# Performance work log

Hardware: AMD Instinct MI355X
Metric: run time of the kernel (lower is better)

## Reference

```python
import jax, jax.numpy as jnp
import numpy as np

N = 100_000          # nodes
E = 800_000          # edges
IN_DIM = 128
OUT_DIM = 128
H = 8                # heads
DK = OUT_DIM // H    # 16
T = 3                # node types
R = 8                # edge relation types
LN_EPS = 1e-5


def setup_inputs():
    key = jax.random.key(0)
    k = jax.random.split(key, 16)
    node_inp = jax.random.normal(k[0], (N, IN_DIM), dtype=jnp.float32)
    node_type = jax.random.randint(k[1], (N,), 0, T)
    edge_index = jax.random.randint(k[2], (2, E), 0, N)
    edge_type = jax.random.randint(k[3], (E,), 0, R)
    edge_sign = jax.random.randint(k[4], (E,), 0, 3) - 1      # values in {-1,0,1}
    edge_distance = jax.random.uniform(k[5], (E,), dtype=jnp.float32) * 2e5
    sc = 1.0 / np.sqrt(IN_DIM)
    Wq = jax.random.normal(k[6], (T, IN_DIM, OUT_DIM), dtype=jnp.float32) * sc
    Wk = jax.random.normal(k[7], (T, IN_DIM, OUT_DIM), dtype=jnp.float32) * sc
    Wv = jax.random.normal(k[8], (T, IN_DIM, OUT_DIM), dtype=jnp.float32) * sc
    bq = jnp.zeros((T, OUT_DIM), jnp.float32)
    bk = jnp.zeros((T, OUT_DIM), jnp.float32)
    bv = jnp.zeros((T, OUT_DIM), jnp.float32)
    rel_q = jax.random.normal(k[9], (R, H, DK), dtype=jnp.float32) * 0.2
    rel_k = jax.random.normal(k[10], (R, H, DK), dtype=jnp.float32) * 0.2
    rel_v = jax.random.normal(k[11], (R, H, DK), dtype=jnp.float32) * 0.2
    rel_bias = jnp.zeros((R, H), jnp.float32)
    ones = jnp.ones((H, DK), dtype=jnp.float32)
    sign_k_fixed = jnp.stack([-ones, ones], axis=0)   # [2,H,DK] buffers (neg,pos)
    sign_v_fixed = jnp.stack([-ones, ones], axis=0)
    sign_k_neutral = jnp.ones((H, DK), jnp.float32)
    sign_v_neutral = jnp.ones((H, DK), jnp.float32)
    dist_alpha = jnp.float32(0.1)
    dist_tau = jnp.float32(1e5)
    skip = jnp.ones((T,), jnp.float32)
    ln_gamma = jnp.ones((T, OUT_DIM), jnp.float32)
    ln_beta = jnp.zeros((T, OUT_DIM), jnp.float32)
    return dict(node_inp=node_inp, node_type=node_type, edge_index=edge_index,
                edge_type=edge_type, edge_sign=edge_sign, edge_distance=edge_distance,
                Wq=Wq, bq=bq, Wk=Wk, bk=bk, Wv=Wv, bv=bv,
                rel_q=rel_q, rel_k=rel_k, rel_v=rel_v, rel_bias=rel_bias,
                sign_k_fixed=sign_k_fixed, sign_v_fixed=sign_v_fixed,
                sign_k_neutral=sign_k_neutral, sign_v_neutral=sign_v_neutral,
                dist_alpha=dist_alpha, dist_tau=dist_tau, skip=skip,
                ln_gamma=ln_gamma, ln_beta=ln_beta)


def reference(node_inp, node_type, edge_index, edge_type, edge_sign, edge_distance,
              Wq, bq, Wk, bk, Wv, bv, rel_q, rel_k, rel_v, rel_bias,
              sign_k_fixed, sign_v_fixed, sign_k_neutral, sign_v_neutral,
              dist_alpha, dist_tau, skip, ln_gamma, ln_beta):
    src, dst = edge_index[0], edge_index[1]
    n = node_inp.shape[0]
    e = src.shape[0]
    # Per-node-type Q/K/V: compute projections for all types [N,T,O], select by type
    # (equivalent to the masked per-type Linear dispatch in the torch code).
    ar = jnp.arange(n)
    Q = (jnp.einsum('nd,tdo->nto', node_inp, Wq) + bq)[ar, node_type].reshape(n, H, DK)
    K = (jnp.einsum('nd,tdo->nto', node_inp, Wk) + bk)[ar, node_type].reshape(n, H, DK)
    V = (jnp.einsum('nd,tdo->nto', node_inp, Wv) + bv)[ar, node_type].reshape(n, H, DK)
    # sign dispatch: -1 -> 0 (neg), +1 -> 1 (pos), anything else -> 2 (neutral)
    sign_idx = jnp.where(edge_sign == -1, 0, jnp.where(edge_sign == 1, 1, 2))
    sign_k_all = jnp.concatenate([sign_k_fixed, sign_k_neutral[None]], axis=0)  # [3,H,DK]
    sign_v_all = jnp.concatenate([sign_v_fixed, sign_v_neutral[None]], axis=0)
    # edge-wise gather + relational modulation
    q_eff = Q[dst] * rel_q[edge_type]                               # [E,H,DK]
    k_eff = K[src] * rel_k[edge_type] * sign_k_all[sign_idx]
    v_eff = V[src] * rel_v[edge_type] * sign_v_all[sign_idx]
    scores = jnp.sum(q_eff * k_eff, axis=-1) / np.sqrt(DK)          # [E,H]
    scores = scores + rel_bias[edge_type]
    phi = dist_alpha * jnp.exp(-edge_distance / (dist_tau + 1e-9))
    scores = scores + phi[:, None]
    # segment softmax over destination nodes
    m = jax.ops.segment_max(scores, dst, num_segments=n)            # [N,H]
    m = jax.lax.stop_gradient(jnp.where(jnp.isfinite(m), m, 0.0))
    es = jnp.exp(scores - m[dst])
    Z = jax.ops.segment_sum(es, dst, num_segments=n)
    attn = es / (Z[dst] + 1e-9)
    # message scatter-aggregate
    msg = (v_eff * attn[:, :, None]).reshape(e, OUT_DIM)
    out = jax.ops.segment_sum(msg, dst, num_segments=n)             # [N,OUT_DIM]
    # per-type gated residual + per-type LayerNorm
    alpha = jax.nn.sigmoid(skip)[node_type][:, None]
    x = alpha * out + (1.0 - alpha) * node_inp
    mu = jnp.mean(x, axis=-1, keepdims=True)
    var = jnp.mean((x - mu) ** 2, axis=-1, keepdims=True)
    xn = (x - mu) * jax.lax.rsqrt(var + LN_EPS)
    return xn * ln_gamma[node_type] + ln_beta[node_type]
```

## Files before the change

### kernel.cpp

```cpp
#include <hip/hip_runtime.h>
#include <hip/hip_bf16.h>

typedef unsigned int uint;
typedef unsigned short ushort;
typedef unsigned long long ull;
typedef __attribute__((ext_vector_type(8))) short short8;
typedef __attribute__((ext_vector_type(4))) float f32x4;

#define WP_ELEMS 147456

__device__ __forceinline__ ushort f2bf(float f) {
  uint x = __float_as_uint(f);
  return (ushort)((x + 0x7fffu + ((x >> 16) & 1u)) >> 16);
}
__device__ __forceinline__ uint packbf(float a, float b) {
  return ((uint)f2bf(b) << 16) | (uint)f2bf(a);
}
__device__ __forceinline__ float bflo(uint u) { return __uint_as_float(u << 16); }
__device__ __forceinline__ float bfhi(uint u) { return __uint_as_float(u & 0xffff0000u); }

__global__ __launch_bounds__(256) void setup_kernel(
    const float* __restrict__ wq, const float* __restrict__ wk, const float* __restrict__ wv,
    const float* __restrict__ rq, const float* __restrict__ rk, const float* __restrict__ rv,
    ushort* __restrict__ Wp, float* __restrict__ ktab, float* __restrict__ vtab,
    const int* __restrict__ ntype, int* __restrict__ cnt,
    const int* __restrict__ edst, int* __restrict__ ecnt, int N, int E) {
  int i = blockIdx.x * 256 + threadIdx.x;
  if (i < WP_ELEMS) {
    int j    = i & 7;
    int lane = (i >> 3) & 63;
    int ot   = (i >> 9) & 7;
    int ks   = (i >> 12) & 3;
    int mt   = i >> 14;
    int mat  = mt / 3;
    int t    = mt - mat * 3;
    int o = ot * 16 + (lane & 15);
    int d = ks * 32 + (lane >> 4) * 8 + j;
    const float* src = (mat == 0) ? wq : (mat == 1) ? wk : wv;
    Wp[i] = f2bf(src[t * 16384 + d * 128 + o]);
  }
  if (i < 1024) {
    ktab[i] = 0.25f * rq[i] * rk[i];
    vtab[i] = rv[i];
  }
  {
    int lane = threadIdx.x & 63;
    int t = (i < N) ? ntype[i] : -1;
#pragma unroll
    for (int tt = 0; tt < 3; ++tt) {
      ull mask = __ballot(t == tt);
      if (mask) {
        int leader = __ffsll((long long)mask) - 1;
        if (lane == leader) atomicAdd(&cnt[tt], __popcll(mask));
      }
    }
  }
  if (i < E) atomicAdd(&ecnt[edst[i]], 1);
}

__global__ void offs_kernel(const int* __restrict__ cnt, int* __restrict__ off) {
  int o = 0;
  off[0] = 0;
  for (int t = 0; t < 3; ++t) {
    o += ((cnt[t] + 63) >> 6) << 6;
    off[t + 1] = o;
  }
}

__global__ __launch_bounds__(256) void fill_kernel(const int* __restrict__ ntype,
                                                   const int* __restrict__ off,
                                                   int* __restrict__ pos,
                                                   int* __restrict__ perm,
                                                   int* __restrict__ pinv, int N) {
  int i = blockIdx.x * 256 + threadIdx.x;
  int lane = threadIdx.x & 63;
  int t = (i < N) ? ntype[i] : -1;
#pragma unroll
  for (int tt = 0; tt < 3; ++tt) {
    ull mask = __ballot(t == tt);
    if (mask) {
      int leader = __ffsll((long long)mask) - 1;
      int base = 0;
      if (lane == leader) base = atomicAdd(&pos[tt], __popcll(mask));
      base = __shfl(base, leader);
      if (t == tt) {
        int rank = __popcll(mask & ((lane == 63) ? 0x7fffffffffffffffull
                                                 : ((1ull << lane) - 1ull)));
        int p = off[tt] + base + rank;
        perm[p] = i;
        pinv[i] = p;
      }
    }
  }
}

__global__ __launch_bounds__(256) void gemm_kernel(
    const float* __restrict__ X, const int* __restrict__ perm,
    const int* __restrict__ off, const ushort* __restrict__ Wp,
    const float* __restrict__ bq, const float* __restrict__ bk, const float* __restrict__ bv,
    float* __restrict__ Qp, uint* __restrict__ KVp) {
  __shared__ __align__(16) char smem[33792];
  __shared__ int prow[64];
  ushort* As = (ushort*)smem;
  float* tbuf = (float*)smem;
  const int tid = threadIdx.x;
  const int base = blockIdx.x * 64;
  const int off1 = off[1], off2 = off[2], off3 = off[3];
  if (base >= off3) return;
  const int t = (base >= off1) + (base >= off2);

  if (tid < 64) prow[tid] = perm[base + tid];
  __syncthreads();
#pragma unroll
  for (int pass = 0; pass < 8; ++pass) {
    int row = pass * 8 + (tid >> 5);
    int dw = tid & 31;
    int p = prow[row];
    uint ux = 0u, uy = 0u;
    if (p >= 0) {
      float4 xv = *(const float4*)(X + (size_t)p * 128 + dw * 4);
      ux = packbf(xv.x, xv.y);
      uy = packbf(xv.z, xv.w);
    }
    uint* s = (uint*)smem + row * 68 + dw * 2;
    s[0] = ux; s[1] = uy;
  }
  __syncthreads();

  const int lane = tid & 63;
  const int w = tid >> 6;
  const int m0 = w * 16;
  const int r = lane & 15;
  const int q = lane >> 4;

  short8 afrag[4];
#pragma unroll
  for (int ks = 0; ks < 4; ++ks)
    afrag[ks] = *(const short8*)(As + (m0 + r) * 136 + ks * 32 + q * 8);
  __syncthreads();

  float* tw = tbuf + w * 2112;
  uint4 ksave[4];
#pragma unroll
  for (int mat = 0; mat < 3; ++mat) {
    f32x4 acc[8];
#pragma unroll
    for (int ot = 0; ot < 8; ++ot) acc[ot] = (f32x4){0.f, 0.f, 0.f, 0.f};

    const ushort* wb = Wp + (size_t)(mat * 3 + t) * 16384 + lane * 8;
#pragma unroll
    for (int ks = 0; ks < 4; ++ks) {
      const ushort* wk_ = wb + ks * 4096;
#pragma unroll
      for (int ot = 0; ot < 8; ++ot) {
        short8 b = *(const short8*)(wk_ + ot * 512);
        acc[ot] = __builtin_amdgcn_mfma_f32_16x16x32_bf16(afrag[ks], b, acc[ot], 0, 0, 0);
      }
    }

    const float* bias = (mat == 0) ? bq : (mat == 1) ? bk : bv;
#pragma unroll
    for (int ot = 0; ot < 8; ++ot) {
      float bi = bias[t * 128 + ot * 16 + r];
#pragma unroll
      for (int reg = 0; reg < 4; ++reg)
        tw[(q * 4 + reg) * 132 + ot * 16 + r] = acc[ot][reg] + bi;
    }
    if (mat == 0) {
#pragma unroll
      for (int p = 0; p < 8; ++p) {
        int f = (p * 64 + lane) * 4;
        int row = f >> 7, col = f & 127;
        float4 val = *(const float4*)(tw + row * 132 + col);
        *(float4*)(Qp + (size_t)(base + m0 + row) * 128 + col) = val;
      }
    } else if (mat == 1) {
#pragma unroll
      for (int p = 0; p < 4; ++p) {
        int g = p * 64 + lane;
        int f = g * 8;
        int row = f >> 7, col = f & 127;
        const float* src = tw + row * 132 + col;
        float4 a4 = *(const float4*)(src);
        float4 b4 = *(const float4*)(src + 4);
        uint4 u;
        u.x = packbf(a4.x, a4.y);
        u.y = packbf(a4.z, a4.w);
        u.z = packbf(b4.x, b4.y);
        u.w = packbf(b4.z, b4.w);
        ksave[p] = u;
      }
    } else {
#pragma unroll
      for (int p = 0; p < 4; ++p) {
        int g = p * 64 + lane;
        int f = g * 8;
        int row = f >> 7, col = f & 127;
        const float* src = tw + row * 132 + col;
        float4 a4 = *(const float4*)(src);
        float4 b4 = *(const float4*)(src + 4);
        uint4 v4;
        v4.x = packbf(a4.x, a4.y);
        v4.y = packbf(a4.z, a4.w);
        v4.z = packbf(b4.x, b4.y);
        v4.w = packbf(b4.z, b4.w);
        uint4 w0, w1;
        w0.x = ksave[p].x; w0.y = v4.x; w0.z = ksave[p].y; w0.w = v4.y;
        w1.x = ksave[p].z; w1.y = v4.z; w1.z = ksave[p].w; w1.w = v4.w;
        uint* dstp = KVp + (size_t)(base + m0 + row) * 128 + col;
        *(uint4*)(dstp) = w0;
        *(uint4*)(dstp + 4) = w1;
      }
    }
  }
}

__global__ __launch_bounds__(256) void csum_kernel(const int* __restrict__ ecnt,
                                                   int* __restrict__ csum, int N) {
  __shared__ int s[4];
  int basei = blockIdx.x * 1024;
  int tid = threadIdx.x;
  int v = 0;
#pragma unroll
  for (int k = 0; k < 4; ++k) {
    int i = basei + k * 256 + tid;
    if (i < N) v += ecnt[i];
  }
#pragma unroll
  for (int m = 1; m < 64; m <<= 1) v += __shfl_xor(v, m);
  if ((tid & 63) == 0) s[tid >> 6] = v;
  __syncthreads();
  if (tid == 0) csum[blockIdx.x] = s[0] + s[1] + s[2] + s[3];
}

__global__ __launch_bounds__(1024) void cscan_kernel(const int* __restrict__ csum,
                                                     int* __restrict__ coff,
                                                     int* __restrict__ rowptrN,
                                                     int NC, int E) {
  __shared__ int sd[32];
  int tid = threadIdx.x, lane = tid & 63, w = tid >> 6;
  int v = (tid < NC) ? csum[tid] : 0;
  int x = v;
#pragma unroll
  for (int d = 1; d < 64; d <<= 1) {
    int t = __shfl_up(x, d);
    if (lane >= d) x += t;
  }
  if (lane == 63) sd[w] = x;
  __syncthreads();
  if (w == 0 && lane < 16) {
    int y = sd[lane];
#pragma unroll
    for (int d = 1; d < 16; d <<= 1) {
      int t = __shfl_up(y, d);
      if (lane >= d) y += t;
    }
    sd[16 + lane] = y;
  }
  __syncthreads();
  int excl = ((w > 0) ? sd[16 + w - 1] : 0) + (x - v);
  if (tid < NC) coff[tid] = excl;
  if (tid == 0) rowptrN[0] = E;
}

__global__ __launch_bounds__(1024) void rowptr_kernel(const int* __restrict__ ecnt,
                                                      const int* __restrict__ coff,
                                                      int* __restrict__ rowptr,
                                                      int* __restrict__ cursor, int N) {
  __shared__ int sd[32];
  int basei = blockIdx.x * 1024;
  int tid = threadIdx.x, lane = tid & 63, w = tid >> 6;
  int i = basei + tid;
  int v = (i < N) ? ecnt[i] : 0;
  int x = v;
#pragma unroll
  for (int d = 1; d < 64; d <<= 1) {
    int t = __shfl_up(x, d);
    if (lane >= d) x += t;
  }
  if (lane == 63) sd[w] = x;
  __syncthreads();
  if (w == 0 && lane < 16) {
    int y = sd[lane];
#pragma unroll
    for (int d = 1; d < 16; d <<= 1) {
      int t = __shfl_up(y, d);
      if (lane >= d) y += t;
    }
    sd[16 + lane] = y;
  }
  __syncthreads();
  int excl = coff[blockIdx.x] + ((w > 0) ? sd[16 + w - 1] : 0) + (x - v);
  if (i < N) { rowptr[i] = excl; cursor[i] = excl; }
}

__global__ __launch_bounds__(256) void scatter_kernel(
    const int* __restrict__ esrc, const int* __restrict__ edst,
    const int* __restrict__ etype, const int* __restrict__ esign,
    const float* __restrict__ edist,
    const float* __restrict__ p_alpha, const float* __restrict__ p_tau,
    const int* __restrict__ pinv, int* __restrict__ cursor,
    int* __restrict__ epk_s, float* __restrict__ ephi_s, int E) {
  int e = blockIdx.x * 256 + threadIdx.x;
  if (e >= E) return;
  int dst = edst[e];
  int p = atomicAdd(&cursor[dst], 1);
  int et = etype[e], sg = esign[e];
  int sbit = (sg == -1) ? 1 : 0;
  float parg = fminf(fmaxf(-edist[e] / (p_tau[0] + 1e-9f), -80.f), 0.f);
  epk_s[p] = pinv[esrc[e]] | (et << 18) | (sbit << 21);
  ephi_s[p] = p_alpha[0] * __expf(parg);
}

struct Pass {
  uint4 kv0, kv1;
  float4 t0, t1;
  float4 v0, v1;
  float bias;
  float sgn;
  int valid;
};

__device__ __forceinline__ Pass fetchp(
    int e0, int row1, const int* __restrict__ epk_s, const float* __restrict__ ephi_s,
    const uint* __restrict__ KVp, const float* __restrict__ ktab,
    const float* __restrict__ vtab, const float* __restrict__ rb, int cl) {
  Pass P;
  P.valid = (e0 < row1);
  int e = P.valid ? e0 : (row1 - 1);
  int pk = epk_s[e];
  float phi = ephi_s[e];
  int pe = pk & 0x3ffff;
  int et = (pk >> 18) & 7;
  P.sgn = (pk & (1 << 21)) ? -1.f : 1.f;
  const uint* kvb = KVp + (size_t)pe * 128 + cl * 8;
  P.kv0 = *(const uint4*)(kvb);
  P.kv1 = *(const uint4*)(kvb + 4);
  const float* kb = ktab + et * 128 + cl * 8;
  P.t0 = *(const float4*)(kb);
  P.t1 = *(const float4*)(kb + 4);
  const float* vb = vtab + et * 128 + cl * 8;
  P.v0 = *(const float4*)(vb);
  P.v1 = *(const float4*)(vb + 4);
  P.bias = rb[et * 8 + (cl >> 1)] + phi;
  return P;
}

__device__ __forceinline__ void computep(
    const Pass& P, const float4& q0, const float4& q1, float& z,
    float& a0, float& a1, float& a2, float& a3,
    float& a4, float& a5, float& a6, float& a7) {
  float part = q0.x * (P.t0.x * bflo(P.kv0.x));
  part = fmaf(q0.y, P.t0.y * bfhi(P.kv0.x), part);
  part = fmaf(q0.z, P.t0.z * bflo(P.kv0.z), part);
  part = fmaf(q0.w, P.t0.w * bfhi(P.kv0.z), part);
  part = fmaf(q1.x, P.t1.x * bflo(P.kv1.x), part);
  part = fmaf(q1.y, P.t1.y * bfhi(P.kv1.x), part);
  part = fmaf(q1.z, P.t1.z * bflo(P.kv1.z), part);
  part = fmaf(q1.w, P.t1.w * bfhi(P.kv1.z), part);
  part += __shfl_xor(part, 1);
  float score = fminf(fmaf(P.sgn, part, P.bias), 80.f);
  float es = __expf(score);
  es = P.valid ? es : 0.f;
  z += es;
  float esv = es * P.sgn;
  a0 = fmaf(esv, P.v0.x * bflo(P.kv0.y), a0);
  a1 = fmaf(esv, P.v0.y * bfhi(P.kv0.y), a1);
  a2 = fmaf(esv, P.v0.z * bflo(P.kv0.w), a2);
  a3 = fmaf(esv, P.v0.w * bfhi(P.kv0.w), a3);
  a4 = fmaf(esv, P.v1.x * bflo(P.kv1.y), a4);
  a5 = fmaf(esv, P.v1.y * bfhi(P.kv1.y), a5);
  a6 = fmaf(esv, P.v1.z * bflo(P.kv1.w), a6);
  a7 = fmaf(esv, P.v1.w * bfhi(P.kv1.w), a7);
}

__global__ __launch_bounds__(256) void agg_kernel(
    const float* __restrict__ Qp, const uint* __restrict__ KVp,
    const int* __restrict__ pinv, const int* __restrict__ rowptr,
    const int* __restrict__ epk_s, const float* __restrict__ ephi_s,
    const float* __restrict__ rb, const float* __restrict__ ktab,
    const float* __restrict__ vtab,
    const float* __restrict__ X, const int* __restrict__ ntype,
    const float* __restrict__ skip, const float* __restrict__ gamma,
    const float* __restrict__ beta, float* __restrict__ y, int N) {
  int dst = blockIdx.x * 4 + (threadIdx.x >> 6);
  if (dst >= N) return;
  int lane = threadIdx.x & 63;
  int g = lane >> 4;
  int cl = lane & 15;
  int c0 = cl * 8;

  int pq = pinv[dst];
  int row0 = rowptr[dst], row1 = rowptr[dst + 1];
  const float* qb = Qp + (size_t)pq * 128 + c0;
  float4 q0 = *(const float4*)(qb);
  float4 q1 = *(const float4*)(qb + 4);

  float a0 = 0.f, a1 = 0.f, a2 = 0.f, a3 = 0.f;
  float a4 = 0.f, a5 = 0.f, a6 = 0.f, a7 = 0.f;
  float z = 0.f;

  int deg = row1 - row0;
  if (deg > 0) {
    int np = (deg + 3) >> 2;
    Pass A = fetchp(row0 + g, row1, epk_s, ephi_s, KVp, ktab, vtab, rb, cl);
    int p = 0;
    while (true) {
      if (p + 1 < np) {
        Pass B = fetchp(row0 + (p + 1) * 4 + g, row1, epk_s, ephi_s, KVp, ktab, vtab, rb, cl);
        computep(A, q0, q1, z, a0, a1, a2, a3, a4, a5, a6, a7);
        A = B;
        ++p;
      } else {
        computep(A, q0, q1, z, a0, a1, a2, a3, a4, a5, a6, a7);
        break;
      }
    }
  }

#pragma unroll
  for (int m = 16; m < 64; m <<= 1) {
    a0 += __shfl_xor(a0, m); a1 += __shfl_xor(a1, m);
    a2 += __shfl_xor(a2, m); a3 += __shfl_xor(a3, m);
    a4 += __shfl_xor(a4, m); a5 += __shfl_xor(a5, m);
    a6 += __shfl_xor(a6, m); a7 += __shfl_xor(a7, m);
    z  += __shfl_xor(z, m);
  }

  if (lane < 16) {
    float inv = 1.0f / (z + 1e-9f);
    float o0 = a0 * inv, o1 = a1 * inv, o2 = a2 * inv, o3 = a3 * inv;
    float o4 = a4 * inv, o5 = a5 * inv, o6 = a6 * inv, o7 = a7 * inv;

    int t = ntype[dst];
    float a = 1.0f / (1.0f + __expf(-skip[t]));
    float b = 1.0f - a;
    const float* xb = X + (size_t)dst * 128 + c0;
    float4 x0 = *(const float4*)(xb);
    float4 x1 = *(const float4*)(xb + 4);
    float w0 = a * o0 + b * x0.x, w1 = a * o1 + b * x0.y;
    float w2 = a * o2 + b * x0.z, w3 = a * o3 + b * x0.w;
    float w4 = a * o4 + b * x1.x, w5 = a * o5 + b * x1.y;
    float w6 = a * o6 + b * x1.z, w7 = a * o7 + b * x1.w;

    float sum = w0 + w1 + w2 + w3 + w4 + w5 + w6 + w7;
    float sq = w0 * w0 + w1 * w1 + w2 * w2 + w3 * w3 +
               w4 * w4 + w5 * w5 + w6 * w6 + w7 * w7;
#pragma unroll
    for (int m = 1; m < 16; m <<= 1) {
      sum += __shfl_xor(sum, m);
      sq  += __shfl_xor(sq, m);
    }
    float mean = sum * (1.0f / 128.0f);
    float var = fmaxf(sq * (1.0f / 128.0f) - mean * mean, 0.0f);
    float rstd = rsqrtf(var + 1e-5f);

    const float* gb = gamma + t * 128 + c0;
    const float* bb2 = beta + t * 128 + c0;
    float4 g0 = *(const float4*)(gb);
    float4 g1 = *(const float4*)(gb + 4);
    float4 be0 = *(const float4*)(bb2);
    float4 be1 = *(const float4*)(bb2 + 4);
    float4 r0, r1;
    r0.x = (w0 - mean) * rstd * g0.x + be0.x;
    r0.y = (w1 - mean) * rstd * g0.y + be0.y;
    r0.z = (w2 - mean) * rstd * g0.z + be0.z;
    r0.w = (w3 - mean) * rstd * g0.w + be0.w;
    r1.x = (w4 - mean) * rstd * g1.x + be1.x;
    r1.y = (w5 - mean) * rstd * g1.y + be1.y;
    r1.z = (w6 - mean) * rstd * g1.z + be1.z;
    r1.w = (w7 - mean) * rstd * g1.w + be1.w;
    float* yb = y + (size_t)dst * 128 + c0;
    *(float4*)(yb) = r0;
    *(float4*)(yb + 4) = r1;
  }
}

extern "C" void kernel_launch(void* const* d_in, const int* in_sizes, int n_in,
                              void* d_out, int out_size, void* d_ws, size_t ws_size,
                              hipStream_t stream) {
  const float* X     = (const float*)d_in[0];
  const int*   ntype = (const int*)d_in[1];
  const int*   eidx  = (const int*)d_in[2];
  const int*   etype = (const int*)d_in[3];
  const int*   esign = (const int*)d_in[4];
  const float* edist = (const float*)d_in[5];
  const float* wq = (const float*)d_in[6];
  const float* bq = (const float*)d_in[7];
  const float* wk = (const float*)d_in[8];
  const float* bk = (const float*)d_in[9];
  const float* wv = (const float*)d_in[10];
  const float* bv = (const float*)d_in[11];
  const float* rq = (const float*)d_in[12];
  const float* rk = (const float*)d_in[13];
  const float* rv = (const float*)d_in[14];
  const float* rb = (const float*)d_in[15];

  const int N = in_sizes[1];
  const int E = in_sizes[3];
  const int NP = N + 192;
  const int NC = (N + 1023) / 1024;

  float* ws = (float*)d_ws;
  float* Qp   = ws;
  uint*  KVp  = (uint*)(Qp + (size_t)NP * 128);
  float* ktab = (float*)(KVp + (size_t)NP * 128);
  float* vtab = ktab + 1024;
  ushort* Wp  = (ushort*)(vtab + 1024);
  int* cnt    = (int*)(Wp + WP_ELEMS);
  int* pos    = cnt + 4;
  int* ecnt   = pos + 4;
  int* perm   = ecnt + N;
  int* pinv   = perm + NP;
  int* off    = pinv + N;
  int* rowptr = off + 4;
  int* cursor = rowptr + N + 1;
  int* csum   = cursor + N;
  int* coff   = csum + 1024;
  int* epk_s  = coff + 1024;
  float* ephi_s = (float*)(epk_s + E);

  hipMemsetAsync(cnt, 0, (size_t)(8 + N) * sizeof(int), stream);
  hipMemsetAsync(perm, 0xFF, (size_t)NP * sizeof(int), stream);

  setup_kernel<<<(E + 255) / 256, 256, 0, stream>>>(
      wq, wk, wv, rq, rk, rv, Wp, ktab, vtab, ntype, cnt, eidx + E, ecnt, N, E);
  offs_kernel<<<1, 1, 0, stream>>>(cnt, off);
  fill_kernel<<<(N + 255) / 256, 256, 0, stream>>>(ntype, off, pos, perm, pinv, N);

  csum_kernel<<<NC, 256, 0, stream>>>(ecnt, csum, N);
  cscan_kernel<<<1, 1024, 0, stream>>>(csum, coff, rowptr + N, NC, E);
  rowptr_kernel<<<NC, 1024, 0, stream>>>(ecnt, coff, rowptr, cursor, N);
  scatter_kernel<<<(E + 255) / 256, 256, 0, stream>>>(
      eidx, eidx + E, etype, esign, edist, (const float*)d_in[20], (const float*)d_in[21],
      pinv, cursor, epk_s, ephi_s, E);

  gemm_kernel<<<(N + 255) / 64, 256, 0, stream>>>(X, perm, off, Wp, bq, bk, bv, Qp, KVp);

  agg_kernel<<<(N + 3) / 4, 256, 0, stream>>>(Qp, KVp, pinv, rowptr, epk_s, ephi_s,
                                              rb, ktab, vtab, X, ntype,
                                              (const float*)d_in[22], (const float*)d_in[23],
                                              (const float*)d_in[24], (float*)d_out, N);
}
```

Measured before the change: 529.1 us.

## Pack edge records, deepen gather prefetch, widen agg blocks and epilogue lanes

Stores each edge's packed key and distance term as one int2 record so a single 8-byte load replaces two separate loads. The aggregation loop now prefetches two passes ahead instead of one and holds only the edge record and K/V gather in registers; the per-type ktab/vtab/bias loads move into the compute step. Blocks grow from 4 to 8 destination nodes (512 threads), and the LayerNorm epilogue uses 32 lanes with 4 values each instead of 16 lanes with 8. The deeper prefetch raises register pressure, which may reduce occupancy.

```diff
diff --git a/kernel.cpp b/kernel.cpp
--- a/kernel.cpp
+++ b/kernel.cpp
@@ -300,7 +300,7 @@
     const float* __restrict__ edist,
     const float* __restrict__ p_alpha, const float* __restrict__ p_tau,
     const int* __restrict__ pinv, int* __restrict__ cursor,
-    int* __restrict__ epk_s, float* __restrict__ ephi_s, int E) {
+    int2* __restrict__ erec, int E) {
   int e = blockIdx.x * 256 + threadIdx.x;
   if (e >= E) return;
   int dst = edst[e];
@@ -308,82 +308,82 @@
   int et = etype[e], sg = esign[e];
   int sbit = (sg == -1) ? 1 : 0;
   float parg = fminf(fmaxf(-edist[e] / (p_tau[0] + 1e-9f), -80.f), 0.f);
-  epk_s[p] = pinv[esrc[e]] | (et << 18) | (sbit << 21);
-  ephi_s[p] = p_alpha[0] * __expf(parg);
-}
-
-struct Pass {
+  int2 r;
+  r.x = pinv[esrc[e]] | (et << 18) | (sbit << 21);
+  r.y = __float_as_int(p_alpha[0] * __expf(parg));
+  erec[p] = r;
+}
+
+struct St {
+  int pk;
+  float phi;
   uint4 kv0, kv1;
-  float4 t0, t1;
-  float4 v0, v1;
-  float bias;
-  float sgn;
-  int valid;
 };
 
-__device__ __forceinline__ Pass fetchp(
-    int e0, int row1, const int* __restrict__ epk_s, const float* __restrict__ ephi_s,
-    const uint* __restrict__ KVp, const float* __restrict__ ktab,
-    const float* __restrict__ vtab, const float* __restrict__ rb, int cl) {
-  Pass P;
-  P.valid = (e0 < row1);
-  int e = P.valid ? e0 : (row1 - 1);
-  int pk = epk_s[e];
-  float phi = ephi_s[e];
-  int pe = pk & 0x3ffff;
-  int et = (pk >> 18) & 7;
-  P.sgn = (pk & (1 << 21)) ? -1.f : 1.f;
-  const uint* kvb = KVp + (size_t)pe * 128 + cl * 8;
-  P.kv0 = *(const uint4*)(kvb);
-  P.kv1 = *(const uint4*)(kvb + 4);
-  const float* kb = ktab + et * 128 + cl * 8;
-  P.t0 = *(const float4*)(kb);
-  P.t1 = *(const float4*)(kb + 4);
-  const float* vb = vtab + et * 128 + cl * 8;
-  P.v0 = *(const float4*)(vb);
-  P.v1 = *(const float4*)(vb + 4);
-  P.bias = rb[et * 8 + (cl >> 1)] + phi;
-  return P;
-}
-
-__device__ __forceinline__ void computep(
-    const Pass& P, const float4& q0, const float4& q1, float& z,
+__device__ __forceinline__ St fetchs(
+    int e0, int row1, const int2* __restrict__ erec,
+    const uint* __restrict__ KVp, int cl) {
+  St s;
+  int e = (e0 < row1) ? e0 : (row1 - 1);
+  int2 r = erec[e];
+  s.pk = r.x | ((e0 < row1) ? 0 : (int)0x80000000);
+  s.phi = __int_as_float(r.y);
+  const uint* kvb = KVp + (size_t)(r.x & 0x3ffff) * 128 + cl * 8;
+  s.kv0 = *(const uint4*)(kvb);
+  s.kv1 = *(const uint4*)(kvb + 4);
+  return s;
+}
+
+__device__ __forceinline__ void computes(
+    const St& s, const float* __restrict__ ktab, const float* __restrict__ vtab,
+    const float* __restrict__ rb, int cl,
+    const float4& q0, const float4& q1, float& z,
     float& a0, float& a1, float& a2, float& a3,
     float& a4, float& a5, float& a6, float& a7) {
-  float part = q0.x * (P.t0.x * bflo(P.kv0.x));
-  part = fmaf(q0.y, P.t0.y * bfhi(P.kv0.x), part);
-  part = fmaf(q0.z, P.t0.z * bflo(P.kv0.z), part);
-  part = fmaf(q0.w, P.t0.w * bfhi(P.kv0.z), part);
-  part = fmaf(q1.x, P.t1.x * bflo(P.kv1.x), part);
-  part = fmaf(q1.y, P.t1.y * bfhi(P.kv1.x), part);
-  part = fmaf(q1.z, P.t1.z * bflo(P.kv1.z), part);
-  part = fmaf(q1.w, P.t1.w * bfhi(P.kv1.z), part);
+  int et = (s.pk >> 18) & 7;
+  float sgn = (s.pk & (1 << 21)) ? -1.f : 1.f;
+  const float* kb = ktab + et * 128 + cl * 8;
+  float4 t0 = *(const float4*)(kb);
+  float4 t1 = *(const float4*)(kb + 4);
+  const float* vb = vtab + et * 128 + cl * 8;
+  float4 v0 = *(const float4*)(vb);
+  float4 v1 = *(const float4*)(vb + 4);
+  float bias = rb[et * 8 + (cl >> 1)] + s.phi;
+
+  float part = q0.x * (t0.x * bflo(s.kv0.x));
+  part = fmaf(q0.y, t0.y * bfhi(s.kv0.x), part);
+  part = fmaf(q0.z, t0.z * bflo(s.kv0.z), part);
+  part = fmaf(q0.w, t0.w * bfhi(s.kv0.z), part);
+  part = fmaf(q1.x, t1.x * bflo(s.kv1.x), part);
+  part = fmaf(q1.y, t1.y * bfhi(s.kv1.x), part);
+  part = fmaf(q1.z, t1.z * bflo(s.kv1.z), part);
+  part = fmaf(q1.w, t1.w * bfhi(s.kv1.z), part);
   part += __shfl_xor(part, 1);
-  float score = fminf(fmaf(P.sgn, part, P.bias), 80.f);
+  float score = fminf(fmaf(sgn, part, bias), 80.f);
   float es = __expf(score);
-  es = P.valid ? es : 0.f;
+  es = (s.pk >= 0) ? es : 0.f;
   z += es;
-  float esv = es * P.sgn;
-  a0 = fmaf(esv, P.v0.x * bflo(P.kv0.y), a0);
-  a1 = fmaf(esv, P.v0.y * bfhi(P.kv0.y), a1);
-  a2 = fmaf(esv, P.v0.z * bflo(P.kv0.w), a2);
-  a3 = fmaf(esv, P.v0.w * bfhi(P.kv0.w), a3);
-  a4 = fmaf(esv, P.v1.x * bflo(P.kv1.y), a4);
-  a5 = fmaf(esv, P.v1.y * bfhi(P.kv1.y), a5);
-  a6 = fmaf(esv, P.v1.z * bflo(P.kv1.w), a6);
-  a7 = fmaf(esv, P.v1.w * bfhi(P.kv1.w), a7);
-}
-
-__global__ __launch_bounds__(256) void agg_kernel(
+  float esv = es * sgn;
+  a0 = fmaf(esv, v0.x * bflo(s.kv0.y), a0);
+  a1 = fmaf(esv, v0.y * bfhi(s.kv0.y), a1);
+  a2 = fmaf(esv, v0.z * bflo(s.kv0.w), a2);
+  a3 = fmaf(esv, v0.w * bfhi(s.kv0.w), a3);
+  a4 = fmaf(esv, v1.x * bflo(s.kv1.y), a4);
+  a5 = fmaf(esv, v1.y * bfhi(s.kv1.y), a5);
+  a6 = fmaf(esv, v1.z * bflo(s.kv1.w), a6);
+  a7 = fmaf(esv, v1.w * bfhi(s.kv1.w), a7);
+}
+
+__global__ __launch_bounds__(512) void agg_kernel(
     const float* __restrict__ Qp, const uint* __restrict__ KVp,
     const int* __restrict__ pinv, const int* __restrict__ rowptr,
-    const int* __restrict__ epk_s, const float* __restrict__ ephi_s,
+    const int2* __restrict__ erec,
     const float* __restrict__ rb, const float* __restrict__ ktab,
     const float* __restrict__ vtab,
     const float* __restrict__ X, const int* __restrict__ ntype,
     const float* __restrict__ skip, const float* __restrict__ gamma,
     const float* __restrict__ beta, float* __restrict__ y, int N) {
-  int dst = blockIdx.x * 4 + (threadIdx.x >> 6);
+  int dst = blockIdx.x * 8 + (threadIdx.x >> 6);
   if (dst >= N) return;
   int lane = threadIdx.x & 63;
   int g = lane >> 4;
@@ -403,17 +403,19 @@
   int deg = row1 - row0;
   if (deg > 0) {
     int np = (deg + 3) >> 2;
-    Pass A = fetchp(row0 + g, row1, epk_s, ephi_s, KVp, ktab, vtab, rb, cl);
-    int p = 0;
-    while (true) {
-      if (p + 1 < np) {
-        Pass B = fetchp(row0 + (p + 1) * 4 + g, row1, epk_s, ephi_s, KVp, ktab, vtab, rb, cl);
-        computep(A, q0, q1, z, a0, a1, a2, a3, a4, a5, a6, a7);
+    St A = fetchs(row0 + g, row1, erec, KVp, cl);
+    St B;
+    if (np > 1) B = fetchs(row0 + 4 + g, row1, erec, KVp, cl);
+    for (int p = 0; p < np; ++p) {
+      if (p + 2 < np) {
+        St C = fetchs(row0 + (p + 2) * 4 + g, row1, erec, KVp, cl);
+        computes(A, ktab, vtab, rb, cl, q0, q1, z, a0, a1, a2, a3, a4, a5, a6, a7);
+        A = B; B = C;
+      } else if (p + 1 < np) {
+        computes(A, ktab, vtab, rb, cl, q0, q1, z, a0, a1, a2, a3, a4, a5, a6, a7);
         A = B;
-        ++p;
       } else {
-        computep(A, q0, q1, z, a0, a1, a2, a3, a4, a5, a6, a7);
-        break;
+        computes(A, ktab, vtab, rb, cl, q0, q1, z, a0, a1, a2, a3, a4, a5, a6, a7);
       }
     }
   }
@@ -427,27 +429,26 @@
     z  += __shfl_xor(z, m);
   }
 
-  if (lane < 16) {
+  if (lane < 32) {
+    int half = lane >> 4;
+    int c4 = c0 + half * 4;
+    float s0 = half ? a4 : a0, s1 = half ? a5 : a1;
+    float s2 = half ? a6 : a2, s3 = half ? a7 : a3;
+
     float inv = 1.0f / (z + 1e-9f);
-    float o0 = a0 * inv, o1 = a1 * inv, o2 = a2 * inv, o3 = a3 * inv;
-    float o4 = a4 * inv, o5 = a5 * inv, o6 = a6 * inv, o7 = a7 * inv;
-
     int t = ntype[dst];
     float a = 1.0f / (1.0f + __expf(-skip[t]));
     float b = 1.0f - a;
-    const float* xb = X + (size_t)dst * 128 + c0;
-    float4 x0 = *(const float4*)(xb);
-    float4 x1 = *(const float4*)(xb + 4);
-    float w0 = a * o0 + b * x0.x, w1 = a * o1 + b * x0.y;
-    float w2 = a * o2 + b * x0.z, w3 = a * o3 + b * x0.w;
-    float w4 = a * o4 + b * x1.x, w5 = a * o5 + b * x1.y;
-    float w6 = a * o6 + b * x1.z, w7 = a * o7 + b * x1.w;
-
-    float sum = w0 + w1 + w2 + w3 + w4 + w5 + w6 + w7;
-    float sq = w0 * w0 + w1 * w1 + w2 * w2 + w3 * w3 +
-               w4 * w4 + w5 * w5 + w6 * w6 + w7 * w7;
-#pragma unroll
-    for (int m = 1; m < 16; m <<= 1) {
+    float4 xv = *(const float4*)(X + (size_t)dst * 128 + c4);
+    float w0 = a * (s0 * inv) + b * xv.x;
+    float w1 = a * (s1 * inv) + b * xv.y;
+    float w2 = a * (s2 * inv) + b * xv.z;
+    float w3 = a * (s3 * inv) + b * xv.w;
+
+    float sum = w0 + w1 + w2 + w3;
+    float sq  = w0 * w0 + w1 * w1 + w2 * w2 + w3 * w3;
+#pragma unroll
+    for (int m = 1; m < 32; m <<= 1) {
       sum += __shfl_xor(sum, m);
       sq  += __shfl_xor(sq, m);
     }
@@ -455,24 +456,14 @@
     float var = fmaxf(sq * (1.0f / 128.0f) - mean * mean, 0.0f);
     float rstd = rsqrtf(var + 1e-5f);
 
-    const float* gb = gamma + t * 128 + c0;
-    const float* bb2 = beta + t * 128 + c0;
-    float4 g0 = *(const float4*)(gb);
-    float4 g1 = *(const float4*)(gb + 4);
-    float4 be0 = *(const float4*)(bb2);
-    float4 be1 = *(const float4*)(bb2 + 4);
-    float4 r0, r1;
-    r0.x = (w0 - mean) * rstd * g0.x + be0.x;
-    r0.y = (w1 - mean) * rstd * g0.y + be0.y;
-    r0.z = (w2 - mean) * rstd * g0.z + be0.z;
-    r0.w = (w3 - mean) * rstd * g0.w + be0.w;
-    r1.x = (w4 - mean) * rstd * g1.x + be1.x;
-    r1.y = (w5 - mean) * rstd * g1.y + be1.y;
-    r1.z = (w6 - mean) * rstd * g1.z + be1.z;
-    r1.w = (w7 - mean) * rstd * g1.w + be1.w;
-    float* yb = y + (size_t)dst * 128 + c0;
-    *(float4*)(yb) = r0;
-    *(float4*)(yb + 4) = r1;
+    float4 gm = *(const float4*)(gamma + t * 128 + c4);
+    float4 bt = *(const float4*)(beta + t * 128 + c4);
+    float4 r;
+    r.x = (w0 - mean) * rstd * gm.x + bt.x;
+    r.y = (w1 - mean) * rstd * gm.y + bt.y;
+    r.z = (w2 - mean) * rstd * gm.z + bt.z;
+    r.w = (w3 - mean) * rstd * gm.w + bt.w;
+    *(float4*)(y + (size_t)dst * 128 + c4) = r;
   }
 }
 
@@ -517,8 +508,7 @@
   int* cursor = rowptr + N + 1;
   int* csum   = cursor + N;
   int* coff   = csum + 1024;
-  int* epk_s  = coff + 1024;
-  float* ephi_s = (float*)(epk_s + E);
+  int2* erec  = (int2*)(coff + 1024);
 
   hipMemsetAsync(cnt, 0, (size_t)(8 + N) * sizeof(int), stream);
   hipMemsetAsync(perm, 0xFF, (size_t)NP * sizeof(int), stream);
@@ -533,11 +523,11 @@
   rowptr_kernel<<<NC, 1024, 0, stream>>>(ecnt, coff, rowptr, cursor, N);
   scatter_kernel<<<(E + 255) / 256, 256, 0, stream>>>(
       eidx, eidx + E, etype, esign, edist, (const float*)d_in[20], (const float*)d_in[21],
-      pinv, cursor, epk_s, ephi_s, E);
+      pinv, cursor, erec, E);
 
   gemm_kernel<<<(N + 255) / 64, 256, 0, stream>>>(X, perm, off, Wp, bq, bk, bv, Qp, KVp);
 
-  agg_kernel<<<(N + 3) / 4, 256, 0, stream>>>(Qp, KVp, pinv, rowptr, epk_s, ephi_s,
+  agg_kernel<<<(N + 7) / 8, 512, 0, stream>>>(Qp, KVp, pinv, rowptr, erec,
                                               rb, ktab, vtab, X, ntype,
                                               (const float*)d_in[22], (const float*)d_in[23],
                                               (const float*)d_in[24], (float*)d_out, N);
```

Measured after the change: 532.5 us. No clear change (+0.6%).
